# Kernel optimization log

Hardware: AMD Instinct MI355X
Metric: run time of the kernel (lower is better)

The kernel has to match this reference:

```python
import jax, jax.numpy as jnp
import numpy as np

TEMPERATURE = 0.07

def l2norm(x, eps=1e-12):
    # torch.nn.functional.normalize(dim=1): x / max(||x||, eps)
    n = jnp.sqrt(jnp.sum(x * x, axis=1, keepdims=True))
    return x / jnp.maximum(n, eps)

def setup_inputs() -> dict:
    key = jax.random.key(0)
    ks = jax.random.split(key, 8)
    B, D_in, H, M, Q, NNEG = 1024, 2048, 1024, 256, 65536, 16384
    return {
        "y1": jax.random.normal(ks[0], (B, D_in), dtype=jnp.float32),
        "y2": jax.random.normal(ks[1], (B, D_in), dtype=jnp.float32),
        "W_enc_q": jax.random.normal(ks[2], (D_in, H), dtype=jnp.float32) * 0.02,
        "W_enc_k": jax.random.normal(ks[3], (D_in, H), dtype=jnp.float32) * 0.02,
        "W_proj": jax.random.normal(ks[4], (H, M), dtype=jnp.float32) * 0.02,
        "queue": jax.random.normal(ks[5], (Q, M), dtype=jnp.float32),
        "sample_idx": jax.random.randint(ks[6], (NNEG,), 0, Q, dtype=jnp.int32),
        "write_idx": jnp.arange(B, dtype=jnp.int32),
    }

def reference(y1, y2, W_enc_q, W_enc_k, W_proj, queue, sample_idx, write_idx):
    # query path (trainable)
    q = l2norm((y2 @ W_enc_q) @ W_proj)                 # [B, M]
    # key path (no_grad in original)
    k = jax.lax.stop_gradient(l2norm((y1 @ W_enc_k) @ W_proj))  # [B, M]
    # sample negatives from GPU-resident queue (gather) + normalize
    neg = l2norm(queue[sample_idx])                     # [NNEG, M]
    pos_logits = jnp.sum(q * k, axis=1, keepdims=True)  # [B, 1]
    neg_logits = q @ neg.T                              # [B, NNEG]
    logits = jnp.concatenate([pos_logits, neg_logits], axis=1) / TEMPERATURE
    # cross_entropy with labels == 0
    loss = -jnp.mean(jax.nn.log_softmax(logits, axis=-1)[:, 0])
    # FIFO append modeled as circular-buffer scatter write
    new_queue = queue.at[write_idx].set(k)
    return loss, new_queue
```

## Files before the change

kernel.cpp:

```cpp
#include <hip/hip_runtime.h>
#include <hip/hip_bf16.h>
#include <math.h>
#include <stdint.h>


typedef __attribute__((ext_vector_type(4))) float floatx4;
typedef __attribute__((ext_vector_type(8))) short bf16x8;
typedef __attribute__((ext_vector_type(8))) unsigned short ushort8;

__device__ __forceinline__ unsigned short f2bf(float x) {
    union { float f; unsigned int u; } v; v.f = x;
    unsigned int r = v.u + 0x7FFFu + ((v.u >> 16) & 1u);
    return (unsigned short)(r >> 16);
}

__device__ __forceinline__ void async_cp16(const void* g, void* l) {
    auto gp = reinterpret_cast<const __attribute__((address_space(1))) unsigned int*>(
        reinterpret_cast<uintptr_t>(g));
    auto lp = reinterpret_cast<__attribute__((address_space(3))) unsigned int*>(
        reinterpret_cast<uintptr_t>(l));
    __builtin_amdgcn_global_load_lds(gp, lp, 16, 0, 0);
}

__global__ __launch_bounds__(256) void prep(
    const float4* __restrict__ queue4, float4* __restrict__ newq4, int nCopy,
    const float* __restrict__ y2, const float* __restrict__ y1,
    unsigned short* __restrict__ y2b, unsigned short* __restrict__ y1b,
    const float* __restrict__ Wq, const float* __restrict__ Wk,
    const float* __restrict__ Wp,
    unsigned short* __restrict__ Wqt, unsigned short* __restrict__ Wkt,
    unsigned short* __restrict__ Wpt,
    const float* __restrict__ queue, const int* __restrict__ sidx,
    unsigned short* __restrict__ negb,
    int D, int H, int M) {
    __shared__ unsigned short tile[32][33];
    const int b = blockIdx.x, t = threadIdx.x;
    const int nCastY = 1024;
    const int nTW = (D / 32) * (H / 32);
    const int nTWp = (H / 32) * (M / 32);

    if (b < nCopy) {
        int base = b * 1024 + t;
#pragma unroll
        for (int i = 0; i < 4; ++i) newq4[base + i * 256] = queue4[base + i * 256];
        return;
    }
    int bb = b - nCopy;
    if (bb < 2 * nCastY) {
        const float* in = (bb < nCastY) ? y2 : y1;
        unsigned short* outp = (bb < nCastY) ? y2b : y1b;
        long i = (long)(bb % nCastY) * 256 + t;
        const float4* in4 = (const float4*)in;
        float4 a = in4[i * 2], c = in4[i * 2 + 1];
        ushort8 o;
        o[0] = f2bf(a.x); o[1] = f2bf(a.y); o[2] = f2bf(a.z); o[3] = f2bf(a.w);
        o[4] = f2bf(c.x); o[5] = f2bf(c.y); o[6] = f2bf(c.z); o[7] = f2bf(c.w);
        ((ushort8*)outp)[i] = o;
        return;
    }
    bb -= 2 * nCastY;
    if (bb < 2 * nTW + nTWp) {
        const float* in; unsigned short* outp; int R, C, idx;
        if (bb < nTW)           { in = Wq; outp = Wqt; R = D; C = H; idx = bb; }
        else if (bb < 2 * nTW)  { in = Wk; outp = Wkt; R = D; C = H; idx = bb - nTW; }
        else                    { in = Wp; outp = Wpt; R = H; C = M; idx = bb - 2 * nTW; }
        int cb = C / 32;
        int c0 = (idx % cb) * 32, r0 = (idx / cb) * 32;
        int tx = t & 31, ty = t >> 5;
#pragma unroll
        for (int i = 0; i < 4; ++i)
            tile[ty + i * 8][tx] = f2bf(in[(size_t)(r0 + ty + i * 8) * C + c0 + tx]);
        __syncthreads();
#pragma unroll
        for (int i = 0; i < 4; ++i)
            outp[(size_t)(c0 + ty + i * 8) * R + r0 + tx] = tile[tx][ty + i * 8];
        return;
    }
    bb -= 2 * nTW + nTWp;
    {
        int r = bb * 4 + (t >> 6);
        int lane = t & 63;
        const float4* src = (const float4*)(queue + (size_t)sidx[r] * 256);
        float4 v = src[lane];
        float ss = v.x * v.x + v.y * v.y + v.z * v.z + v.w * v.w;
#pragma unroll
        for (int off = 1; off < 64; off <<= 1) ss += __shfl_xor(ss, off);
        float inv = 1.f / fmaxf(sqrtf(ss), 1e-12f);
        unsigned short o[4] = { f2bf(v.x * inv), f2bf(v.y * inv),
                                f2bf(v.z * inv), f2bf(v.w * inv) };
        *(unsigned long long*)(negb + (size_t)r * 256 + lane * 4) =
            *(unsigned long long*)o;
    }
}

__global__ __launch_bounds__(256) void gemm_enc(const unsigned short* __restrict__ Ag,
                                                const unsigned short* __restrict__ Bg,
                                                unsigned short* __restrict__ Cg,
                                                int No, int Ko,
                                                long sAb, long sBb, long sCb) {
    __shared__ unsigned short As[128 * 32];
    __shared__ unsigned short Bs[64 * 32];
    const int batch = blockIdx.z;
    const unsigned short* A = Ag + (long)batch * sAb;
    const unsigned short* B = Bg + (long)batch * sBb;
    unsigned short* C = Cg + (long)batch * sCb;
    const int row0 = blockIdx.y * 128, col0 = blockIdx.x * 64;
    const int t = threadIdx.x;
    const int lane = t & 63, wave = t >> 6;
    const int wr = wave >> 1, wc = wave & 1;
    const int lrow = lane & 15, quad = lane >> 4;

    floatx4 acc[4][2] = {};

    for (int kk = 0; kk < Ko; kk += 32) {
        {
            int c0 = t, c1 = t + 256;
            async_cp16(A + (size_t)(row0 + (c0 >> 2)) * Ko + kk + (c0 & 3) * 8,
                       (char*)As + (size_t)c0 * 16);
            async_cp16(A + (size_t)(row0 + (c1 >> 2)) * Ko + kk + (c1 & 3) * 8,
                       (char*)As + (size_t)c1 * 16);
            async_cp16(B + (size_t)(col0 + (t >> 2)) * Ko + kk + (t & 3) * 8,
                       (char*)Bs + (size_t)t * 16);
        }
        __syncthreads();
        bf16x8 af[4], bf[2];
#pragma unroll
        for (int i = 0; i < 4; ++i)
            af[i] = *(const bf16x8*)(As + (size_t)(wr * 64 + i * 16 + lrow) * 32 + quad * 8);
#pragma unroll
        for (int j = 0; j < 2; ++j)
            bf[j] = *(const bf16x8*)(Bs + (size_t)(wc * 32 + j * 16 + lrow) * 32 + quad * 8);
#pragma unroll
        for (int i = 0; i < 4; ++i)
#pragma unroll
            for (int j = 0; j < 2; ++j)
                acc[i][j] = __builtin_amdgcn_mfma_f32_16x16x32_bf16(af[i], bf[j], acc[i][j], 0, 0, 0);
        __syncthreads();
    }
#pragma unroll
    for (int i = 0; i < 4; ++i) {
        int grow = row0 + wr * 64 + i * 16 + quad * 4;
#pragma unroll
        for (int j = 0; j < 2; ++j) {
            int gcol = col0 + wc * 32 + j * 16 + lrow;
#pragma unroll
            for (int r = 0; r < 4; ++r)
                C[(size_t)(grow + r) * No + gcol] = f2bf(acc[i][j][r]);
        }
    }
}

__global__ __launch_bounds__(256) void gemm_proj(const unsigned short* __restrict__ Ag,
                                                 const unsigned short* __restrict__ Bg,
                                                 float* __restrict__ Pg,
                                                 int No, int Ko, int nsplit,
                                                 long sAb) {
    __shared__ unsigned short As[128 * 32];
    __shared__ unsigned short Bs[64 * 32];
    const int z = blockIdx.z;
    const int batch = z / nsplit, split = z - batch * nsplit;
    const unsigned short* A = Ag + (long)batch * sAb;
    const unsigned short* B = Bg;
    float* P = Pg + (long)z * 1024 * No;
    const int Kc = Ko / nsplit, kbeg = split * Kc;
    const int row0 = blockIdx.y * 128, col0 = blockIdx.x * 64;
    const int t = threadIdx.x;
    const int lane = t & 63, wave = t >> 6;
    const int wr = wave >> 1, wc = wave & 1;
    const int lrow = lane & 15, quad = lane >> 4;

    floatx4 acc[4][2] = {};

    for (int kk = kbeg; kk < kbeg + Kc; kk += 32) {
        {
            int c0 = t, c1 = t + 256;
            async_cp16(A + (size_t)(row0 + (c0 >> 2)) * Ko + kk + (c0 & 3) * 8,
                       (char*)As + (size_t)c0 * 16);
            async_cp16(A + (size_t)(row0 + (c1 >> 2)) * Ko + kk + (c1 & 3) * 8,
                       (char*)As + (size_t)c1 * 16);
            async_cp16(B + (size_t)(col0 + (t >> 2)) * Ko + kk + (t & 3) * 8,
                       (char*)Bs + (size_t)t * 16);
        }
        __syncthreads();
        bf16x8 af[4], bf[2];
#pragma unroll
        for (int i = 0; i < 4; ++i)
            af[i] = *(const bf16x8*)(As + (size_t)(wr * 64 + i * 16 + lrow) * 32 + quad * 8);
#pragma unroll
        for (int j = 0; j < 2; ++j)
            bf[j] = *(const bf16x8*)(Bs + (size_t)(wc * 32 + j * 16 + lrow) * 32 + quad * 8);
#pragma unroll
        for (int i = 0; i < 4; ++i)
#pragma unroll
            for (int j = 0; j < 2; ++j)
                acc[i][j] = __builtin_amdgcn_mfma_f32_16x16x32_bf16(af[i], bf[j], acc[i][j], 0, 0, 0);
        __syncthreads();
    }
#pragma unroll
    for (int i = 0; i < 4; ++i) {
        int grow = row0 + wr * 64 + i * 16 + quad * 4;
#pragma unroll
        for (int j = 0; j < 2; ++j) {
            int gcol = col0 + wc * 32 + j * 16 + lrow;
#pragma unroll
            for (int r = 0; r < 4; ++r)
                P[(size_t)(grow + r) * No + gcol] = acc[i][j][r];
        }
    }
}

__global__ __launch_bounds__(256) void qk_finalize(const float* __restrict__ P,
                                                   const int* __restrict__ widx,
                                                   unsigned short* __restrict__ qkb,
                                                   float* __restrict__ newq,
                                                   float* __restrict__ pos,
                                                   float* __restrict__ sumexp,
                                                   int B_, int nsplit, float invT) {
    const int i = blockIdx.x, t = threadIdx.x;
    const long RM = (long)B_ * 256;
    float sq = 0.f, sk = 0.f;
    for (int s = 0; s < nsplit; ++s) {
        sq += P[(long)s * RM + (long)i * 256 + t];
        sk += P[(long)(nsplit + s) * RM + (long)i * 256 + t];
    }
    __shared__ float r0[256], r1[256], r2[256];
    r0[t] = sq * sq; r1[t] = sk * sk; r2[t] = sq * sk;
    __syncthreads();
    for (int off = 128; off > 0; off >>= 1) {
        if (t < off) { r0[t] += r0[t + off]; r1[t] += r1[t + off]; r2[t] += r2[t + off]; }
        __syncthreads();
    }
    float nq = fmaxf(sqrtf(r0[0]), 1e-12f);
    float nk = fmaxf(sqrtf(r1[0]), 1e-12f);
    float qn = sq / nq, kn = sk / nk;
    qkb[(size_t)i * 256 + t] = f2bf(qn);
    qkb[(size_t)(B_ + i) * 256 + t] = f2bf(kn);
    newq[(size_t)widx[i] * 256 + t] = kn;
    if (t == 0) {
        float p = (r2[0] / (nq * nk)) * invT;
        pos[i] = p;
        sumexp[i] = __expf(p);
    }
}

__global__ __launch_bounds__(256) void gemm_logits(const unsigned short* __restrict__ A,
                                                   const unsigned short* __restrict__ B,
                                                   float* __restrict__ sumexp,
                                                   int Ko, float invT) {
    __shared__ unsigned short As[128 * 64];
    __shared__ unsigned short Bs[128 * 64];
    __shared__ float rowred[128];
    const int row0 = blockIdx.y * 128, col0 = blockIdx.x * 128;
    const int t = threadIdx.x;
    const int lane = t & 63, wave = t >> 6;
    const int wr = wave >> 1, wc = wave & 1;
    const int lrow = lane & 15, quad = lane >> 4;

    floatx4 acc[4][4] = {};

    for (int kk = 0; kk < Ko; kk += 64) {
#pragma unroll
        for (int r = 0; r < 4; ++r) {
            int c = t + r * 256;
            async_cp16(A + (size_t)(row0 + (c >> 3)) * Ko + kk + (c & 7) * 8,
                       (char*)As + (size_t)c * 16);
            async_cp16(B + (size_t)(col0 + (c >> 3)) * Ko + kk + (c & 7) * 8,
                       (char*)Bs + (size_t)c * 16);
        }
        __syncthreads();
        bf16x8 af[4][2], bf[4][2];
#pragma unroll
        for (int i = 0; i < 4; ++i)
#pragma unroll
            for (int k2 = 0; k2 < 2; ++k2) {
                af[i][k2] = *(const bf16x8*)(As + (size_t)(wr * 64 + i * 16 + lrow) * 64 + k2 * 32 + quad * 8);
                bf[i][k2] = *(const bf16x8*)(Bs + (size_t)(wc * 64 + i * 16 + lrow) * 64 + k2 * 32 + quad * 8);
            }
#pragma unroll
        for (int k2 = 0; k2 < 2; ++k2)
#pragma unroll
            for (int i = 0; i < 4; ++i)
#pragma unroll
                for (int j = 0; j < 4; ++j)
                    acc[i][j] = __builtin_amdgcn_mfma_f32_16x16x32_bf16(af[i][k2], bf[j][k2], acc[i][j], 0, 0, 0);
        __syncthreads();
    }
    if (t < 128) rowred[t] = 0.f;
    __syncthreads();
#pragma unroll
    for (int i = 0; i < 4; ++i) {
#pragma unroll
        for (int r = 0; r < 4; ++r) {
            float s = 0.f;
#pragma unroll
            for (int j = 0; j < 4; ++j) s += __expf(acc[i][j][r] * invT);
            s += __shfl_xor(s, 1); s += __shfl_xor(s, 2);
            s += __shfl_xor(s, 4); s += __shfl_xor(s, 8);
            if (lrow == 0) atomicAdd(&rowred[wr * 64 + i * 16 + quad * 4 + r], s);
        }
    }
    __syncthreads();
    if (t < 128) atomicAdd(&sumexp[row0 + t], rowred[t]);
}

__global__ __launch_bounds__(256) void final_loss(const float* __restrict__ pos,
                                                  const float* __restrict__ sumexp,
                                                  float* __restrict__ out, int B_) {
    const int t = threadIdx.x;
    float acc = 0.f;
    for (int i = t; i < B_; i += 256) acc += logf(sumexp[i]) - pos[i];
    __shared__ float s[256];
    s[t] = acc;
    __syncthreads();
    for (int off = 128; off > 0; off >>= 1) {
        if (t < off) s[t] += s[t + off];
        __syncthreads();
    }
    if (t == 0) out[0] = s[0] / (float)B_;
}

extern "C" void kernel_launch(void* const* d_in, const int* in_sizes, int n_in,
                              void* d_out, int out_size, void* d_ws, size_t ws_size,
                              hipStream_t stream) {
    const float* y1    = (const float*)d_in[0];
    const float* y2    = (const float*)d_in[1];
    const float* Wq    = (const float*)d_in[2];
    const float* Wk    = (const float*)d_in[3];
    const float* Wp    = (const float*)d_in[4];
    const float* queue = (const float*)d_in[5];
    const int*   sidx  = (const int*)d_in[6];
    const int*   widx  = (const int*)d_in[7];
    float* out = (float*)d_out;

    const int B    = in_sizes[7];
    const int NNEG = in_sizes[6];
    const int D    = in_sizes[0] / B;
    const int H    = in_sizes[2] / D;
    const int M    = in_sizes[4] / H;
    const int Q    = in_sizes[5] / M;
    const float invT = 1.0f / 0.07f;
    const int NS_P = 4;

    float* ws  = (float*)d_ws;
    float* Pp     = ws;
    float* pos    = Pp + (size_t)2 * NS_P * B * M;
    float* sumexp = pos + B;
    unsigned short* us = (unsigned short*)(sumexp + B);
    unsigned short* y2b  = us;
    unsigned short* y1b  = y2b + (size_t)B * D;
    unsigned short* Wqt  = y1b + (size_t)B * D;
    unsigned short* Wkt  = Wqt + (size_t)H * D;
    unsigned short* Wpt  = Wkt + (size_t)H * D;
    unsigned short* T12b = Wpt + (size_t)M * H;
    unsigned short* qkb  = T12b + (size_t)2 * B * H;
    unsigned short* negb = qkb + (size_t)2 * B * M;

    const int nCopy = (int)((size_t)Q * M / 4 / 1024);
    const int nPrep = nCopy + 2 * 1024 + 2 * (D / 32) * (H / 32)
                    + (H / 32) * (M / 32) + NNEG / 4;
    prep<<<nPrep, 256, 0, stream>>>((const float4*)queue, (float4*)(out + 1), nCopy,
                                    y2, y1, y2b, y1b, Wq, Wk, Wp, Wqt, Wkt, Wpt,
                                    queue, sidx, negb, D, H, M);

    gemm_enc<<<dim3(H / 64, B / 128, 2), 256, 0, stream>>>(
        y2b, Wqt, T12b, H, D, (long)B * D, (long)H * D, (long)B * H);

    gemm_proj<<<dim3(M / 64, B / 128, 2 * NS_P), 256, 0, stream>>>(
        T12b, Wpt, Pp, M, H, NS_P, (long)B * H);

    qk_finalize<<<B, 256, 0, stream>>>(Pp, widx, qkb, out + 1, pos, sumexp,
                                       B, NS_P, invT);

    gemm_logits<<<dim3(NNEG / 128, B / 128), 256, 0, stream>>>(
        qkb, negb, sumexp, M, invT);

    final_loss<<<1, 256, 0, stream>>>(pos, sumexp, out, B);
}
```

Baseline: 239.8 us.

## Co-schedule queue copy and negative gather with encoder GEMM in one launch

```diff
diff --git a/kernel.cpp b/kernel.cpp
--- a/kernel.cpp
+++ b/kernel.cpp
@@ -22,34 +22,23 @@
     __builtin_amdgcn_global_load_lds(gp, lp, 16, 0, 0);
 }
 
-__global__ __launch_bounds__(256) void prep(
-    const float4* __restrict__ queue4, float4* __restrict__ newq4, int nCopy,
+__global__ __launch_bounds__(256) void prep_small(
     const float* __restrict__ y2, const float* __restrict__ y1,
     unsigned short* __restrict__ y2b, unsigned short* __restrict__ y1b,
     const float* __restrict__ Wq, const float* __restrict__ Wk,
     const float* __restrict__ Wp,
     unsigned short* __restrict__ Wqt, unsigned short* __restrict__ Wkt,
     unsigned short* __restrict__ Wpt,
-    const float* __restrict__ queue, const int* __restrict__ sidx,
-    unsigned short* __restrict__ negb,
     int D, int H, int M) {
     __shared__ unsigned short tile[32][33];
     const int b = blockIdx.x, t = threadIdx.x;
     const int nCastY = 1024;
     const int nTW = (D / 32) * (H / 32);
-    const int nTWp = (H / 32) * (M / 32);
-
-    if (b < nCopy) {
-        int base = b * 1024 + t;
-#pragma unroll
-        for (int i = 0; i < 4; ++i) newq4[base + i * 256] = queue4[base + i * 256];
-        return;
-    }
-    int bb = b - nCopy;
-    if (bb < 2 * nCastY) {
-        const float* in = (bb < nCastY) ? y2 : y1;
-        unsigned short* outp = (bb < nCastY) ? y2b : y1b;
-        long i = (long)(bb % nCastY) * 256 + t;
+
+    if (b < 2 * nCastY) {
+        const float* in = (b < nCastY) ? y2 : y1;
+        unsigned short* outp = (b < nCastY) ? y2b : y1b;
+        long i = (long)(b % nCastY) * 256 + t;
         const float4* in4 = (const float4*)in;
         float4 a = in4[i * 2], c = in4[i * 2 + 1];
         ushort8 o;
@@ -58,95 +47,104 @@
         ((ushort8*)outp)[i] = o;
         return;
     }
-    bb -= 2 * nCastY;
-    if (bb < 2 * nTW + nTWp) {
-        const float* in; unsigned short* outp; int R, C, idx;
-        if (bb < nTW)           { in = Wq; outp = Wqt; R = D; C = H; idx = bb; }
-        else if (bb < 2 * nTW)  { in = Wk; outp = Wkt; R = D; C = H; idx = bb - nTW; }
-        else                    { in = Wp; outp = Wpt; R = H; C = M; idx = bb - 2 * nTW; }
-        int cb = C / 32;
-        int c0 = (idx % cb) * 32, r0 = (idx / cb) * 32;
-        int tx = t & 31, ty = t >> 5;
-#pragma unroll
-        for (int i = 0; i < 4; ++i)
-            tile[ty + i * 8][tx] = f2bf(in[(size_t)(r0 + ty + i * 8) * C + c0 + tx]);
-        __syncthreads();
-#pragma unroll
-        for (int i = 0; i < 4; ++i)
-            outp[(size_t)(c0 + ty + i * 8) * R + r0 + tx] = tile[tx][ty + i * 8];
-        return;
-    }
-    bb -= 2 * nTW + nTWp;
-    {
-        int r = bb * 4 + (t >> 6);
-        int lane = t & 63;
-        const float4* src = (const float4*)(queue + (size_t)sidx[r] * 256);
-        float4 v = src[lane];
-        float ss = v.x * v.x + v.y * v.y + v.z * v.z + v.w * v.w;
-#pragma unroll
-        for (int off = 1; off < 64; off <<= 1) ss += __shfl_xor(ss, off);
-        float inv = 1.f / fmaxf(sqrtf(ss), 1e-12f);
-        unsigned short o[4] = { f2bf(v.x * inv), f2bf(v.y * inv),
-                                f2bf(v.z * inv), f2bf(v.w * inv) };
-        *(unsigned long long*)(negb + (size_t)r * 256 + lane * 4) =
-            *(unsigned long long*)o;
-    }
-}
-
-__global__ __launch_bounds__(256) void gemm_enc(const unsigned short* __restrict__ Ag,
-                                                const unsigned short* __restrict__ Bg,
-                                                unsigned short* __restrict__ Cg,
-                                                int No, int Ko,
-                                                long sAb, long sBb, long sCb) {
+    int bb = b - 2 * nCastY;
+    const float* in; unsigned short* outp; int R, C, idx;
+    if (bb < nTW)           { in = Wq; outp = Wqt; R = D; C = H; idx = bb; }
+    else if (bb < 2 * nTW)  { in = Wk; outp = Wkt; R = D; C = H; idx = bb - nTW; }
+    else                    { in = Wp; outp = Wpt; R = H; C = M; idx = bb - 2 * nTW; }
+    int cb = C / 32;
+    int c0 = (idx % cb) * 32, r0 = (idx / cb) * 32;
+    int tx = t & 31, ty = t >> 5;
+#pragma unroll
+    for (int i = 0; i < 4; ++i)
+        tile[ty + i * 8][tx] = f2bf(in[(size_t)(r0 + ty + i * 8) * C + c0 + tx]);
+    __syncthreads();
+#pragma unroll
+    for (int i = 0; i < 4; ++i)
+        outp[(size_t)(c0 + ty + i * 8) * R + r0 + tx] = tile[tx][ty + i * 8];
+}
+
+__global__ __launch_bounds__(256) void enc_plus(
+    const unsigned short* __restrict__ Yb,
+    const unsigned short* __restrict__ Wt,
+    unsigned short* __restrict__ T12b,
+    const float4* __restrict__ queue4, float4* __restrict__ newq4,
+    const float* __restrict__ queue, const int* __restrict__ sidx,
+    unsigned short* __restrict__ negb) {
     __shared__ unsigned short As[128 * 32];
     __shared__ unsigned short Bs[64 * 32];
-    const int batch = blockIdx.z;
-    const unsigned short* A = Ag + (long)batch * sAb;
-    const unsigned short* B = Bg + (long)batch * sBb;
-    unsigned short* C = Cg + (long)batch * sCb;
-    const int row0 = blockIdx.y * 128, col0 = blockIdx.x * 64;
-    const int t = threadIdx.x;
-    const int lane = t & 63, wave = t >> 6;
-    const int wr = wave >> 1, wc = wave & 1;
-    const int lrow = lane & 15, quad = lane >> 4;
-
-    floatx4 acc[4][2] = {};
-
-    for (int kk = 0; kk < Ko; kk += 32) {
-        {
+    const int b = blockIdx.x, t = threadIdx.x;
+    const int type = b % 7, id = b / 7;
+
+    if (type == 0) {
+        const int batch = id >> 7, rem = id & 127;
+        const int col0 = (rem & 15) * 64, row0 = (rem >> 4) * 128;
+        const unsigned short* A = Yb + (long)batch * 1024 * 2048;
+        const unsigned short* Bp = Wt + (long)batch * 1024 * 2048;
+        unsigned short* C = T12b + (long)batch * 1024 * 1024;
+        const int Ko = 2048, No = 1024;
+        const int lane = t & 63, wave = t >> 6;
+        const int wr = wave >> 1, wc = wave & 1;
+        const int lrow = lane & 15, quad = lane >> 4;
+
+        floatx4 acc[4][2] = {};
+        for (int kk = 0; kk < Ko; kk += 32) {
             int c0 = t, c1 = t + 256;
             async_cp16(A + (size_t)(row0 + (c0 >> 2)) * Ko + kk + (c0 & 3) * 8,
                        (char*)As + (size_t)c0 * 16);
             async_cp16(A + (size_t)(row0 + (c1 >> 2)) * Ko + kk + (c1 & 3) * 8,
                        (char*)As + (size_t)c1 * 16);
-            async_cp16(B + (size_t)(col0 + (t >> 2)) * Ko + kk + (t & 3) * 8,
+            async_cp16(Bp + (size_t)(col0 + (t >> 2)) * Ko + kk + (t & 3) * 8,
                        (char*)Bs + (size_t)t * 16);
-        }
-        __syncthreads();
-        bf16x8 af[4], bf[2];
-#pragma unroll
-        for (int i = 0; i < 4; ++i)
-            af[i] = *(const bf16x8*)(As + (size_t)(wr * 64 + i * 16 + lrow) * 32 + quad * 8);
-#pragma unroll
-        for (int j = 0; j < 2; ++j)
-            bf[j] = *(const bf16x8*)(Bs + (size_t)(wc * 32 + j * 16 + lrow) * 32 + quad * 8);
-#pragma unroll
-        for (int i = 0; i < 4; ++i)
+            __syncthreads();
+            bf16x8 af[4], bf[2];
+#pragma unroll
+            for (int i = 0; i < 4; ++i)
+                af[i] = *(const bf16x8*)(As + (size_t)(wr * 64 + i * 16 + lrow) * 32 + quad * 8);
 #pragma unroll
             for (int j = 0; j < 2; ++j)
-                acc[i][j] = __builtin_amdgcn_mfma_f32_16x16x32_bf16(af[i], bf[j], acc[i][j], 0, 0, 0);
-        __syncthreads();
-    }
-#pragma unroll
-    for (int i = 0; i < 4; ++i) {
-        int grow = row0 + wr * 64 + i * 16 + quad * 4;
-#pragma unroll
-        for (int j = 0; j < 2; ++j) {
-            int gcol = col0 + wc * 32 + j * 16 + lrow;
-#pragma unroll
-            for (int r = 0; r < 4; ++r)
-                C[(size_t)(grow + r) * No + gcol] = f2bf(acc[i][j][r]);
-        }
+                bf[j] = *(const bf16x8*)(Bs + (size_t)(wc * 32 + j * 16 + lrow) * 32 + quad * 8);
+#pragma unroll
+            for (int i = 0; i < 4; ++i)
+#pragma unroll
+                for (int j = 0; j < 2; ++j)
+                    acc[i][j] = __builtin_amdgcn_mfma_f32_16x16x32_bf16(af[i], bf[j], acc[i][j], 0, 0, 0);
+            __syncthreads();
+        }
+#pragma unroll
+        for (int i = 0; i < 4; ++i) {
+            int grow = row0 + wr * 64 + i * 16 + quad * 4;
+#pragma unroll
+            for (int j = 0; j < 2; ++j) {
+                int gcol = col0 + wc * 32 + j * 16 + lrow;
+#pragma unroll
+                for (int r = 0; r < 4; ++r)
+                    C[(size_t)(grow + r) * No + gcol] = f2bf(acc[i][j][r]);
+            }
+        }
+    } else if (type == 3 || type == 6) {
+        const int gid = id * 2 + (type == 6);
+        const int w = t >> 6, lane = t & 63;
+#pragma unroll
+        for (int j = 0; j < 8; ++j) {
+            int r = gid * 32 + w * 8 + j;
+            const float4* src = (const float4*)(queue + (size_t)sidx[r] * 256);
+            float4 v = src[lane];
+            float ss = v.x * v.x + v.y * v.y + v.z * v.z + v.w * v.w;
+#pragma unroll
+            for (int off = 1; off < 64; off <<= 1) ss += __shfl_xor(ss, off);
+            float inv = 1.f / fmaxf(sqrtf(ss), 1e-12f);
+            unsigned short o[4] = { f2bf(v.x * inv), f2bf(v.y * inv),
+                                    f2bf(v.z * inv), f2bf(v.w * inv) };
+            *(unsigned long long*)(negb + (size_t)r * 256 + lane * 4) =
+                *(unsigned long long*)o;
+        }
+    } else {
+        const int cid = id * 4 + (type - 1 - (type > 3));
+        int base = cid * 4096 + t;
+#pragma unroll
+        for (int i = 0; i < 16; ++i)
+            newq4[base + i * 256] = queue4[base + i * 256];
     }
 }
 
@@ -172,15 +170,13 @@
     floatx4 acc[4][2] = {};
 
     for (int kk = kbeg; kk < kbeg + Kc; kk += 32) {
-        {
-            int c0 = t, c1 = t + 256;
-            async_cp16(A + (size_t)(row0 + (c0 >> 2)) * Ko + kk + (c0 & 3) * 8,
-                       (char*)As + (size_t)c0 * 16);
-            async_cp16(A + (size_t)(row0 + (c1 >> 2)) * Ko + kk + (c1 & 3) * 8,
-                       (char*)As + (size_t)c1 * 16);
-            async_cp16(B + (size_t)(col0 + (t >> 2)) * Ko + kk + (t & 3) * 8,
-                       (char*)Bs + (size_t)t * 16);
-        }
+        int c0 = t, c1 = t + 256;
+        async_cp16(A + (size_t)(row0 + (c0 >> 2)) * Ko + kk + (c0 & 3) * 8,
+                   (char*)As + (size_t)c0 * 16);
+        async_cp16(A + (size_t)(row0 + (c1 >> 2)) * Ko + kk + (c1 & 3) * 8,
+                   (char*)As + (size_t)c1 * 16);
+        async_cp16(B + (size_t)(col0 + (t >> 2)) * Ko + kk + (t & 3) * 8,
+                   (char*)Bs + (size_t)t * 16);
         __syncthreads();
         bf16x8 af[4], bf[2];
 #pragma unroll
@@ -355,15 +351,13 @@
     unsigned short* qkb  = T12b + (size_t)2 * B * H;
     unsigned short* negb = qkb + (size_t)2 * B * M;
 
-    const int nCopy = (int)((size_t)Q * M / 4 / 1024);
-    const int nPrep = nCopy + 2 * 1024 + 2 * (D / 32) * (H / 32)
-                    + (H / 32) * (M / 32) + NNEG / 4;
-    prep<<<nPrep, 256, 0, stream>>>((const float4*)queue, (float4*)(out + 1), nCopy,
-                                    y2, y1, y2b, y1b, Wq, Wk, Wp, Wqt, Wkt, Wpt,
-                                    queue, sidx, negb, D, H, M);
-
-    gemm_enc<<<dim3(H / 64, B / 128, 2), 256, 0, stream>>>(
-        y2b, Wqt, T12b, H, D, (long)B * D, (long)H * D, (long)B * H);
+    const int nPrep = 2 * 1024 + 2 * (D / 32) * (H / 32) + (H / 32) * (M / 32);
+    prep_small<<<nPrep, 256, 0, stream>>>(y2, y1, y2b, y1b, Wq, Wk, Wp,
+                                          Wqt, Wkt, Wpt, D, H, M);
+
+    enc_plus<<<1792, 256, 0, stream>>>(y2b, Wqt, T12b,
+                                       (const float4*)queue, (float4*)(out + 1),
+                                       queue, sidx, negb);
 
     gemm_proj<<<dim3(M / 64, B / 128, 2 * NS_P), 256, 0, stream>>>(
         T12b, Wpt, Pp, M, H, NS_P, (long)B * H);
```

New measurement: 232.7 us. 1.03x faster.
